# Performance work log

Measured on AMD Instinct MI355X. Metric: run time of the kernel, lower is better.

## Reference

```python
import jax, jax.numpy as jnp
import numpy as np

N, E = 50000, 800000
IN, HID, OUT, HEADS = 128, 64, 32, 2


def setup_inputs() -> dict:
    key = jax.random.key(0)
    ks = jax.random.split(key, 16)
    def w(k, shape, fan_in):
        return jax.random.normal(k, shape, dtype=jnp.float32) / np.sqrt(fan_in).astype(np.float32)
    x = jax.random.normal(ks[0], (N, IN), dtype=jnp.float32)
    edge_index = jax.random.randint(ks[1], (2, E), 0, N)
    return {
        "x": x,
        "edge_index": edge_index,
        # GCNConv 1: in -> hid
        "W1": w(ks[2], (IN, HID), IN), "b1": jnp.zeros((HID,), jnp.float32),
        # GCNConv 2: hid -> hid
        "W2": w(ks[3], (HID, HID), HID), "b2": jnp.zeros((HID,), jnp.float32),
        # GATConv 1: hid -> hid, heads=2, concat=True
        "Wg1": w(ks[4], (HID, HEADS * HID), HID),
        "asrc1": w(ks[5], (HEADS, HID), HID), "adst1": w(ks[6], (HEADS, HID), HID),
        "bg1": jnp.zeros((HEADS * HID,), jnp.float32),
        # GATConv 2: hid*2 -> out, heads=2, concat=False (mean over heads)
        "Wg2": w(ks[7], (HEADS * HID, HEADS * OUT), HEADS * HID),
        "asrc2": w(ks[8], (HEADS, OUT), OUT), "adst2": w(ks[9], (HEADS, OUT), OUT),
        "bg2": jnp.zeros((OUT,), jnp.float32),
    }


def _add_self_loops(edge_index, n):
    loop = jnp.arange(n, dtype=edge_index.dtype)
    src = jnp.concatenate([edge_index[0], loop])
    dst = jnp.concatenate([edge_index[1], loop])
    return src, dst


def _gcn_conv(x, W, b, src, dst, n):
    # PyG GCNConv: symmetric normalization with self-loops (already appended).
    h = x @ W  # [N, C]
    deg = jax.ops.segment_sum(jnp.ones(src.shape, jnp.float32), dst, num_segments=n)
    dinv = jnp.where(deg > 0, jax.lax.rsqrt(deg), 0.0)
    norm = dinv[src] * dinv[dst]                       # [E']
    out = jax.ops.segment_sum(h[src] * norm[:, None], dst, num_segments=n)
    return out + b


def _gat_conv(x, W, a_src, a_dst, bias, src, dst, n, heads, ch, concat):
    # PyG GATConv: per-edge LeakyReLU score, softmax over incoming edges of dst.
    h = (x @ W).reshape(n, heads, ch)                  # [N, H, C]
    s = jnp.sum(h * a_src, axis=-1)                    # [N, H]
    d = jnp.sum(h * a_dst, axis=-1)                    # [N, H]
    e = jax.nn.leaky_relu(s[src] + d[dst], negative_slope=0.2)  # [E', H]
    m = jax.ops.segment_max(e, dst, num_segments=n)    # segment-softmax, stable
    a = jnp.exp(e - m[dst])
    z = jax.ops.segment_sum(a, dst, num_segments=n)
    a = a / (z[dst] + 1e-16)
    out = jax.ops.segment_sum(h[src] * a[:, :, None], dst, num_segments=n)  # [N, H, C]
    out = out.reshape(n, heads * ch) if concat else out.mean(axis=1)
    return out + bias


def reference(x, edge_index, W1, b1, W2, b2, Wg1, asrc1, adst1, bg1, Wg2, asrc2, adst2, bg2):
    n = x.shape[0]
    src, dst = _add_self_loops(edge_index, n)
    h = jax.nn.relu(_gcn_conv(x, W1, b1, src, dst, n))
    h = jax.nn.relu(_gcn_conv(h, W2, b2, src, dst, n))
    h = jax.nn.relu(_gat_conv(h, Wg1, asrc1, adst1, bg1, src, dst, n, HEADS, HID, True))
    h = _gat_conv(h, Wg2, asrc2, adst2, bg2, src, dst, n, HEADS, OUT, False)
    return jax.nn.log_softmax(h, axis=1)
```

## Files before the change

kernel.cpp:

```cpp
#include <hip/hip_runtime.h>
#include <hip/hip_bf16.h>

typedef __hip_bfloat16 bf16;
typedef __attribute__((ext_vector_type(8))) short bf16x8;
typedef __attribute__((ext_vector_type(4))) float f32x4;

constexpr int NN = 50000;
constexpr int NE = 800000;
constexpr int NT = NE + NN;
constexpr int NNB  = (NN + 127)/128;
constexpr int NPART = 8;
constexpr int PCAP = 512;

__device__ __forceinline__ float cvt(const void* p, long long i, int f32){
  return f32 ? ((const float*)p)[i] : __bfloat162float(((const bf16*)p)[i]);
}
__device__ __forceinline__ unsigned short f2bf(float f){
  unsigned u = __float_as_uint(f);
  u += 0x7fffu + ((u >> 16) & 1);
  return (unsigned short)(u >> 16);
}
__device__ __forceinline__ float bflo(unsigned p){ return __uint_as_float(p << 16); }
__device__ __forceinline__ float bfhi(unsigned p){ return __uint_as_float(p & 0xffff0000u); }
__device__ __forceinline__ unsigned packbf(float a, float b){
  return (unsigned)f2bf(a) | ((unsigned)f2bf(b) << 16);
}
__device__ __forceinline__ unsigned f2key(float f){
  unsigned u = __float_as_uint(f);
  return (u & 0x80000000u) ? ~u : (u | 0x80000000u);
}
__device__ __forceinline__ float key2f(unsigned k){
  unsigned u = (k & 0x80000000u) ? (k & 0x7fffffffu) : ~k;
  return __uint_as_float(u);
}

struct SrcPtrs { const void* p[12]; };
__global__ void k_cvtall(SrcPtrs sp, float* __restrict__ Wc,
                         unsigned short* __restrict__ Wf, int* __restrict__ flag){
  const int sz[12]  = {8192,64,4096,64,8192,128,128,128,8192,64,64,32};
  const int off[12] = {0,8192,8256,12352,12416,20608,20736,20864,20992,29184,29248,29312};
  __shared__ int bad;
  int tid = threadIdx.x;
  if(tid == 0) bad = 0;
  __syncthreads();
  const unsigned short* q = (const unsigned short*)sp.p[0];
  int local = 0;
  for(int i = tid; i < 8192; i += 256){
    int e = (q[i] >> 7) & 0xFF;
    if(e >= 0xC0) local = 1;
  }
  if(local) atomicOr(&bad, 1);
  __syncthreads();
  int f = bad;
  int b = blockIdx.x;
  if(b == 0 && tid == 0) *flag = f;
  if(b < 12){
    const void* src = sp.p[b];
    float* dst = Wc + off[b];
    int n = sz[b];
    for(int i = tid; i < n; i += 256) dst[i] = cvt(src, i, f);
  } else {
    int g = b - 12;
    const int KK[4]   = {128, 64, 64, 128};
    const int NNo[4]  = {64, 64, 128, 64};
    const int srcI[4] = {0, 2, 4, 8};
    const int foff[4] = {0, 16384, 24576, 40960};
    int K = KK[g], N = NNo[g], KF = K/32;
    const void* src = sp.p[srcI[g]];
    unsigned short* dh = Wf + foff[g];
    unsigned short* dl = dh + K*N;
    int tot = K*N;
    for(int idx = tid; idx < tot; idx += 256){
      int i = idx & 7, lane = (idx >> 3) & 63, fr = idx >> 9;
      int kf = fr % KF, nf = fr / KF;
      int k = kf*32 + ((lane >> 4) << 3) + i;
      int n = nf*16 + (lane & 15);
      float w = cvt(src, (long long)k*N + n, f);
      unsigned short h = f2bf(w);
      dh[idx] = h;
      dl[idx] = f2bf(w - __uint_as_float((unsigned)h << 16));
    }
  }
}

__global__ void k_bin(const int* __restrict__ ei, int* __restrict__ bcur,
                      unsigned* __restrict__ tmp){
  int e = blockIdx.x*256 + threadIdx.x;
  int p = blockIdx.x & (NPART-1);
  if(e < NE){
    int dst = ei[NE + e];
    int src = ei[e];
    int b = dst >> 7;
    int pos = atomicAdd(&bcur[(p*NNB + b)*16], 1);
    if(pos < PCAP) tmp[((size_t)(b*NPART + p) << 9) + pos] = (unsigned)src | ((unsigned)(dst & 127) << 16);
  }
}
__global__ void k_scatter(const int* __restrict__ bcur,
                          const unsigned* __restrict__ tmp, int* __restrict__ rowptr,
                          int* __restrict__ rowend, float* __restrict__ dinv,
                          unsigned short* __restrict__ srcidx16){
  __shared__ int hist[128];
  __shared__ int lcur[128];
  __shared__ int sh[2][128];
  __shared__ int red[256];
  int b = blockIdx.x;
  int dst0 = b << 7;
  int nd = min(128, NN - dst0);
  int tid = threadIdx.x;
  int partial = 0;
  for(int i = tid; i < b*NPART; i += 256){
    int b2 = i >> 3, p = i & 7;
    partial += bcur[(p*NNB + b2)*16];
  }
  red[tid] = partial;
  if(tid < 128) hist[tid] = 0;
  __syncthreads();
  for(int off = 128; off; off >>= 1){
    if(tid < off) red[tid] += red[tid + off];
    __syncthreads();
  }
  int base = red[0] + (b << 7);
  for(int p = 0; p < NPART; p++){
    int cnt = min(bcur[(p*NNB + b)*16], PCAP);
    const unsigned* tp = tmp + ((size_t)(b*NPART + p) << 9);
    for(int i = tid; i < cnt; i += 256) atomicAdd(&hist[tp[i] >> 16], 1);
  }
  __syncthreads();
  int c = (tid < 128) ? hist[tid] + 1 : 0;
  if(tid < 128) sh[0][tid] = c;
  __syncthreads();
  int cur = 0;
  for(int off = 1; off < 128; off <<= 1){
    int nxt = cur^1;
    if(tid < 128){
      int v = sh[cur][tid];
      if(tid >= off) v += sh[cur][tid-off];
      sh[nxt][tid] = v;
    }
    __syncthreads();
    cur = nxt;
  }
  if(tid < nd){
    int rp = base + sh[cur][tid] - c;
    int d = dst0 + tid;
    rowptr[d] = rp;
    srcidx16[rp] = (unsigned short)d;
    rowend[d] = rp + c;
    dinv[d] = rsqrtf((float)c);
    lcur[tid] = rp + 1;
  }
  __syncthreads();
  for(int p = 0; p < NPART; p++){
    int cnt = min(bcur[(p*NNB + b)*16], PCAP);
    const unsigned* tp = tmp + ((size_t)(b*NPART + p) << 9);
    for(int i = tid; i < cnt; i += 256){
      unsigned v = tp[i];
      int pos = atomicAdd(&lcur[v >> 16], 1);
      srcidx16[pos] = (unsigned short)(v & 0xffffu);
    }
  }
}

template<int KIN, int KOUT, bool SCALE, int PACKC, int MODE>
__global__ void k_mfma(const void* __restrict__ X, const unsigned short* __restrict__ Wh,
                       const unsigned short* __restrict__ Wl,
                       const float* __restrict__ dinv, void* __restrict__ out,
                       const float* __restrict__ asrc, const float* __restrict__ adst,
                       float* __restrict__ sS, float* __restrict__ sD,
                       unsigned* __restrict__ ska, const int* __restrict__ flag){
  constexpr int KF = KIN/32;
  constexpr int NF = KOUT/16;
  constexpr int PITCH = KOUT + 1;
  __shared__ float Cl[64*PITCH];
  __shared__ unsigned skey[2];
  int tid = threadIdx.x;
  if(PACKC > 0 && tid < 2) skey[tid] = 0;
  int wv = tid >> 6, lane = tid & 63;
  int lr = lane >> 4, lc = lane & 15;
  int row0 = blockIdx.x*64;
  int arow = row0 + wv*16 + lc;
  if(arow >= NN) arow = NN - 1;
  int f = (MODE == 1) ? *flag : 0;
  const char* xb = (const char*)X;
  f32x4 acc[NF];
#pragma unroll
  for(int nf = 0; nf < NF; nf++) acc[nf] = (f32x4){0.f,0.f,0.f,0.f};
#pragma unroll
  for(int kf = 0; kf < KF; kf++){
    bf16x8 a;
    if(MODE == 1 && f){
      const float* xf = (const float*)xb + (size_t)arow*KIN + kf*32 + lr*8;
      float4 u = *(const float4*)xf;
      float4 v = *(const float4*)(xf + 4);
      a[0]=(short)f2bf(u.x); a[1]=(short)f2bf(u.y); a[2]=(short)f2bf(u.z); a[3]=(short)f2bf(u.w);
      a[4]=(short)f2bf(v.x); a[5]=(short)f2bf(v.y); a[6]=(short)f2bf(v.z); a[7]=(short)f2bf(v.w);
    } else {
      a = *(const bf16x8*)(xb + (size_t)arow*(KIN*2) + kf*64 + lr*16);
    }
#pragma unroll
    for(int nf = 0; nf < NF; nf++){
      int fr = nf*KF + kf;
      bf16x8 wh = *(const bf16x8*)((const short*)Wh + (fr << 9) + (lane << 3));
      bf16x8 wl = *(const bf16x8*)((const short*)Wl + (fr << 9) + (lane << 3));
      acc[nf] = __builtin_amdgcn_mfma_f32_16x16x32_bf16(a, wh, acc[nf], 0, 0, 0);
      acc[nf] = __builtin_amdgcn_mfma_f32_16x16x32_bf16(a, wl, acc[nf], 0, 0, 0);
    }
  }
#pragma unroll
  for(int nf = 0; nf < NF; nf++)
#pragma unroll
    for(int r = 0; r < 4; r++)
      Cl[(wv*16 + lr*4 + r)*PITCH + nf*16 + lc] = acc[nf][r];
  __syncthreads();
  int row = tid >> 2, q = tid & 3;
  int grow = row0 + row;
  bool valid = grow < NN;
  const float* cr = &Cl[row*PITCH];
  if constexpr (PACKC == 0){
    float s = SCALE ? (valid ? dinv[grow] : 0.0f) : 1.0f;
    unsigned ov[8];
#pragma unroll
    for(int j = 0; j < 8; j++)
      ov[j] = packbf(cr[q*16 + 2*j]*s, cr[q*16 + 2*j + 1]*s);
    if(valid){
      unsigned* op = (unsigned*)out + (size_t)grow*(KOUT/2) + q*8;
      *(uint4*)op       = make_uint4(ov[0],ov[1],ov[2],ov[3]);
      *(uint4*)(op + 4) = make_uint4(ov[4],ov[5],ov[6],ov[7]);
    }
  } else {
    constexpr int C = PACKC;
    constexpr int CT = C/4;
    float s0=0.f, d0=0.f, s1=0.f, d1=0.f;
    unsigned ov[CT];
#pragma unroll
    for(int j = 0; j < CT; j++){
      int c = q*CT + j;
      float a = cr[c], bb = cr[C + c];
      ov[j] = packbf(a, bb);
      s0 += a*asrc[c];      d0 += a*adst[c];
      s1 += bb*asrc[C + c]; d1 += bb*adst[C + c];
    }
    if(valid){
      unsigned* op = (unsigned*)out + (size_t)grow*C + q*CT;
#pragma unroll
      for(int j4 = 0; j4 < CT/4; j4++)
        *(uint4*)(op + 4*j4) = make_uint4(ov[4*j4],ov[4*j4+1],ov[4*j4+2],ov[4*j4+3]);
    }
    s0 += __shfl_xor(s0,1); s0 += __shfl_xor(s0,2);
    d0 += __shfl_xor(d0,1); d0 += __shfl_xor(d0,2);
    s1 += __shfl_xor(s1,1); s1 += __shfl_xor(s1,2);
    d1 += __shfl_xor(d1,1); d1 += __shfl_xor(d1,2);
    if(valid && q == 0){
      *(float2*)(sS + 2*grow) = make_float2(s0, s1);
      *(float2*)(sD + 2*grow) = make_float2(d0, d1);
      atomicMax(&skey[0], f2key(s0));
      atomicMax(&skey[1], f2key(s1));
    }
    __syncthreads();
    if(tid < 2) atomicMax(&ska[tid*32 + (blockIdx.x & 31)], skey[tid]);
  }
}

__global__ void k_gcn_gather(const int* __restrict__ rowptr, const int* __restrict__ rowend,
                             const unsigned short* __restrict__ srcidx16, const float* __restrict__ dinv,
                             const unsigned* __restrict__ Au32, const float* __restrict__ bias,
                             unsigned* __restrict__ B){
  int wid = threadIdx.x >> 6, lane = threadIdx.x & 63;
  int n = blockIdx.x*4 + wid;
  if(n >= NN) return;
  int s0 = rowptr[n], ne = rowend[n] - s0;
  int o = lane >> 3, c4 = lane & 7;
  float a0=0,a1=0,a2=0,a3=0,a4=0,a5=0,a6=0,a7=0;
  for(int base = 0; base < ne; base += 64){
    int my = base + lane;
    int src = (my < ne) ? (int)srcidx16[s0 + my] : -1;
    int cnt = min(64, ne - base);
    int iters = (cnt + 7) >> 3;
#pragma unroll 4
    for(int j = 0; j < iters; j++){
      int sb = __shfl(src, 8*j + o);
      if(sb >= 0){
        uint4 p = *(const uint4*)(Au32 + (size_t)sb*32 + c4*4);
        a0 += bflo(p.x); a1 += bfhi(p.x);
        a2 += bflo(p.y); a3 += bfhi(p.y);
        a4 += bflo(p.z); a5 += bfhi(p.z);
        a6 += bflo(p.w); a7 += bfhi(p.w);
      }
    }
  }
#pragma unroll
  for(int off = 8; off <= 32; off <<= 1){
    a0 += __shfl_xor(a0, off); a1 += __shfl_xor(a1, off);
    a2 += __shfl_xor(a2, off); a3 += __shfl_xor(a3, off);
    a4 += __shfl_xor(a4, off); a5 += __shfl_xor(a5, off);
    a6 += __shfl_xor(a6, off); a7 += __shfl_xor(a7, off);
  }
  if(o == 0){
    float dn = dinv[n];
    int cb = 8*c4;
    uint4 r;
    r.x = packbf(fmaxf(a0*dn + bias[cb+0], 0.0f), fmaxf(a1*dn + bias[cb+1], 0.0f));
    r.y = packbf(fmaxf(a2*dn + bias[cb+2], 0.0f), fmaxf(a3*dn + bias[cb+3], 0.0f));
    r.z = packbf(fmaxf(a4*dn + bias[cb+4], 0.0f), fmaxf(a5*dn + bias[cb+5], 0.0f));
    r.w = packbf(fmaxf(a6*dn + bias[cb+6], 0.0f), fmaxf(a7*dn + bias[cb+7], 0.0f));
    *(uint4*)(B + (size_t)n*32 + c4*4) = r;
  }
}

__device__ __forceinline__ void ska_max2(const unsigned* __restrict__ ska, int lane,
                                         float& m0, float& m1){
  unsigned kk = ska[lane];
#pragma unroll
  for(int off = 1; off <= 16; off <<= 1) kk = max(kk, __shfl_xor(kk, off));
  m0 = key2f(__shfl(kk, 0));
  m1 = key2f(__shfl(kk, 32));
}

__global__ void k_gat1_gather(const int* __restrict__ rowptr, const int* __restrict__ rowend,
                              const unsigned short* __restrict__ srcidx16, const float* __restrict__ sS,
                              const float* __restrict__ sD, const unsigned* __restrict__ Ab,
                              const float* __restrict__ bias, unsigned* __restrict__ B,
                              const unsigned* __restrict__ ska){
  int wid = threadIdx.x >> 6, lane = threadIdx.x & 63;
  int n = blockIdx.x*4 + wid;
  if(n >= NN) return;
  float g0, g1;
  ska_max2(ska, lane, g0, g1);
  int s0 = rowptr[n], ne = rowend[n] - s0;
  float d0 = sD[n*2], d1 = sD[n*2+1];
  float t0 = g0 + d0;  float m0 = t0 > 0.0f ? t0 : 0.2f*t0;
  float t1 = g1 + d1;  float m1 = t1 > 0.0f ? t1 : 0.2f*t1;
  int q = lane >> 4, c4 = lane & 15;
  float z0 = 0.0f, z1 = 0.0f;
  float b0=0,b1=0,b2=0,b3=0, c0=0,c1=0,c2=0,c3=0;
  for(int base = 0; base < ne; base += 64){
    int my = base + lane;
    int src = 0; float w0 = 0.0f, w1 = 0.0f;
    if(my < ne){
      src = (int)srcidx16[s0 + my];
      float2 sv = *(const float2*)(sS + src*2);
      float e0 = sv.x + d0; e0 = e0 > 0.0f ? e0 : 0.2f*e0;
      float e1 = sv.y + d1; e1 = e1 > 0.0f ? e1 : 0.2f*e1;
      w0 = __expf(e0 - m0); w1 = __expf(e1 - m1);
      z0 += w0; z1 += w1;
    }
    int cnt = min(64, ne - base);
    int iters = (cnt + 3) >> 2;
#pragma unroll 4
    for(int j = 0; j < iters; j++){
      int idx = 4*j + q;
      int sb = __shfl(src, idx);
      float a0 = __shfl(w0, idx), a1 = __shfl(w1, idx);
      uint4 p = *(const uint4*)(Ab + (size_t)sb*64 + c4*4);
      b0 += bflo(p.x)*a0; c0 += bfhi(p.x)*a1;
      b1 += bflo(p.y)*a0; c1 += bfhi(p.y)*a1;
      b2 += bflo(p.z)*a0; c2 += bfhi(p.z)*a1;
      b3 += bflo(p.w)*a0; c3 += bfhi(p.w)*a1;
    }
  }
#pragma unroll
  for(int off = 1; off <= 32; off <<= 1){ z0 += __shfl_xor(z0, off); z1 += __shfl_xor(z1, off); }
#pragma unroll
  for(int off = 16; off <= 32; off <<= 1){
    b0 += __shfl_xor(b0, off); b1 += __shfl_xor(b1, off);
    b2 += __shfl_xor(b2, off); b3 += __shfl_xor(b3, off);
    c0 += __shfl_xor(c0, off); c1 += __shfl_xor(c1, off);
    c2 += __shfl_xor(c2, off); c3 += __shfl_xor(c3, off);
  }
  if(q == 0){
    float iz0 = 1.0f/(z0 + 1e-16f), iz1 = 1.0f/(z1 + 1e-16f);
    int cb = 4*c4;
    uint2 r0, r1;
    r0.x = packbf(fmaxf(b0*iz0 + bias[cb+0], 0.0f), fmaxf(b1*iz0 + bias[cb+1], 0.0f));
    r0.y = packbf(fmaxf(b2*iz0 + bias[cb+2], 0.0f), fmaxf(b3*iz0 + bias[cb+3], 0.0f));
    r1.x = packbf(fmaxf(c0*iz1 + bias[64+cb+0], 0.0f), fmaxf(c1*iz1 + bias[64+cb+1], 0.0f));
    r1.y = packbf(fmaxf(c2*iz1 + bias[64+cb+2], 0.0f), fmaxf(c3*iz1 + bias[64+cb+3], 0.0f));
    *(uint2*)(B + (size_t)n*64 + 2*c4)      = r0;
    *(uint2*)(B + (size_t)n*64 + 32 + 2*c4) = r1;
  }
}

__global__ void k_gat2_final(const int* __restrict__ rowptr, const int* __restrict__ rowend,
                             const unsigned short* __restrict__ srcidx16, const float* __restrict__ sS,
                             const float* __restrict__ sD, const unsigned* __restrict__ Ab,
                             const float* __restrict__ bias, void* __restrict__ out,
                             const int* __restrict__ flag, const unsigned* __restrict__ ska){
  int wid = threadIdx.x >> 6, lane = threadIdx.x & 63;
  int n = blockIdx.x*4 + wid;
  if(n >= NN) return;
  float g0, g1;
  ska_max2(ska, lane, g0, g1);
  int s0 = rowptr[n], ne = rowend[n] - s0;
  float d0 = sD[n*2], d1 = sD[n*2+1];
  float t0 = g0 + d0;  float m0 = t0 > 0.0f ? t0 : 0.2f*t0;
  float t1 = g1 + d1;  float m1 = t1 > 0.0f ? t1 : 0.2f*t1;
  int o = lane >> 3, c4 = lane & 7;
  float z0 = 0.0f, z1 = 0.0f;
  float b0=0,b1=0,b2=0,b3=0, c0=0,c1=0,c2=0,c3=0;
  for(int base = 0; base < ne; base += 64){
    int my = base + lane;
    int src = 0; float w0 = 0.0f, w1 = 0.0f;
    if(my < ne){
      src = (int)srcidx16[s0 + my];
      float2 sv = *(const float2*)(sS + src*2);
      float e0 = sv.x + d0; e0 = e0 > 0.0f ? e0 : 0.2f*e0;
      float e1 = sv.y + d1; e1 = e1 > 0.0f ? e1 : 0.2f*e1;
      w0 = __expf(e0 - m0); w1 = __expf(e1 - m1);
      z0 += w0; z1 += w1;
    }
    int cnt = min(64, ne - base);
    int iters = (cnt + 7) >> 3;
#pragma unroll 4
    for(int j = 0; j < iters; j++){
      int idx = 8*j + o;
      int sb = __shfl(src, idx);
      float a0 = __shfl(w0, idx), a1 = __shfl(w1, idx);
      uint4 p = *(const uint4*)(Ab + (size_t)sb*32 + c4*4);
      b0 += bflo(p.x)*a0; c0 += bfhi(p.x)*a1;
      b1 += bflo(p.y)*a0; c1 += bfhi(p.y)*a1;
      b2 += bflo(p.z)*a0; c2 += bfhi(p.z)*a1;
      b3 += bflo(p.w)*a0; c3 += bfhi(p.w)*a1;
    }
  }
#pragma unroll
  for(int off = 1; off <= 32; off <<= 1){ z0 += __shfl_xor(z0, off); z1 += __shfl_xor(z1, off); }
#pragma unroll
  for(int off = 8; off <= 32; off <<= 1){
    b0 += __shfl_xor(b0, off); b1 += __shfl_xor(b1, off);
    b2 += __shfl_xor(b2, off); b3 += __shfl_xor(b3, off);
    c0 += __shfl_xor(c0, off); c1 += __shfl_xor(c1, off);
    c2 += __shfl_xor(c2, off); c3 += __shfl_xor(c3, off);
  }
  float iz0 = 1.0f/(z0 + 1e-16f), iz1 = 1.0f/(z1 + 1e-16f);
  int cb = 4*c4;
  float o0 = 0.5f*(b0*iz0 + c0*iz1) + bias[cb+0];
  float o1 = 0.5f*(b1*iz0 + c1*iz1) + bias[cb+1];
  float o2 = 0.5f*(b2*iz0 + c2*iz1) + bias[cb+2];
  float o3 = 0.5f*(b3*iz0 + c3*iz1) + bias[cb+3];
  float mx = fmaxf(fmaxf(o0, o1), fmaxf(o2, o3));
  for(int off = 4; off; off >>= 1) mx = fmaxf(mx, __shfl_xor(mx, off));
  float sm = __expf(o0 - mx) + __expf(o1 - mx) + __expf(o2 - mx) + __expf(o3 - mx);
  for(int off = 4; off; off >>= 1) sm += __shfl_xor(sm, off);
  float lse = mx + __logf(sm);
  if(o == 0){
    if(*flag){
      float4 r;
      r.x = o0 - lse; r.y = o1 - lse; r.z = o2 - lse; r.w = o3 - lse;
      *(float4*)((float*)out + (size_t)n*32 + cb) = r;
    } else {
      uint2 r;
      r.x = packbf(o0 - lse, o1 - lse);
      r.y = packbf(o2 - lse, o3 - lse);
      *(uint2*)((unsigned*)out + (size_t)n*16 + 2*c4) = r;
    }
  }
}

extern "C" void kernel_launch(void* const* d_in, const int* in_sizes, int n_in,
                              void* d_out, int out_size, void* d_ws, size_t ws_size,
                              hipStream_t stream) {
  const void* x   = d_in[0];
  const int*  ei  = (const int*)d_in[1];

  float* A    = (float*)d_ws;
  unsigned short* Au = (unsigned short*)A;
  unsigned* Au32 = (unsigned*)A;
  unsigned* Ab = (unsigned*)(A + (size_t)NN*64);
  float* B    = A + (size_t)NN*128;
  float* dinv = B + (size_t)NN*128;
  float* sS   = dinv + NN;
  float* sD   = sS + 2*NN;
  int* rowptr = (int*)(sD + 2*NN);
  int* rowend = rowptr + NN;
  unsigned short* srcidx16 = (unsigned short*)(rowend + NN);
  unsigned* SKA = (unsigned*)(srcidx16 + NT + 2);
  int* bcur   = (int*)(SKA + 128);
  unsigned* tmp = (unsigned*)(bcur + NPART*NNB*16);
  float* Wc   = (float*)(tmp + (size_t)NNB*NPART*PCAP);
  int*  flag  = (int*)(Wc + 29344);
  uintptr_t wfp = ((uintptr_t)(flag + 1) + 15) & ~(uintptr_t)15;
  unsigned short* Wf = (unsigned short*)wfp;

  const float* b1c  = Wc + 8192;
  const float* b2c  = Wc + 12352;
  const float* as1c = Wc + 20608;
  const float* ad1c = Wc + 20736;
  const float* bg1c = Wc + 20864;
  const float* as2c = Wc + 29184;
  const float* ad2c = Wc + 29248;
  const float* bg2c = Wc + 29312;

  auto nb = [](long long t){ return dim3((unsigned)((t + 255)/256)); };
  dim3 gnodes((NN + 3)/4);
  dim3 g64((NN + 63)/64);

  SrcPtrs sp;
  for(int i = 0; i < 12; i++) sp.p[i] = d_in[2 + i];
  k_cvtall<<<16, 256, 0, stream>>>(sp, Wc, Wf, flag);

  (void)hipMemsetAsync(SKA, 0, 512 + NPART*NNB*16*4, stream);

  k_bin<<<nb(NE), 256, 0, stream>>>(ei, bcur, tmp);
  k_scatter<<<NNB, 256, 0, stream>>>(bcur, tmp, rowptr, rowend, dinv, srcidx16);

  k_mfma<128,64,true,0,1><<<g64, 256, 0, stream>>>(
      x, Wf, Wf + 8192, dinv, Au, nullptr, nullptr, nullptr, nullptr, nullptr, flag);
  k_gcn_gather<<<gnodes, 256, 0, stream>>>(rowptr, rowend, srcidx16, dinv, Au32, b1c, (unsigned*)B);

  k_mfma<64,64,true,0,0><<<g64, 256, 0, stream>>>(
      B, Wf + 16384, Wf + 20480, dinv, Au, nullptr, nullptr, nullptr, nullptr, nullptr, flag);
  k_gcn_gather<<<gnodes, 256, 0, stream>>>(rowptr, rowend, srcidx16, dinv, Au32, b2c, (unsigned*)B);

  k_mfma<64,128,false,64,0><<<g64, 256, 0, stream>>>(
      B, Wf + 24576, Wf + 32768, dinv, Ab, as1c, ad1c, sS, sD, SKA, flag);
  k_gat1_gather<<<gnodes, 256, 0, stream>>>(rowptr, rowend, srcidx16, sS, sD, Ab, bg1c, (unsigned*)B, SKA);

  k_mfma<128,64,false,32,0><<<g64, 256, 0, stream>>>(
      B, Wf + 40960, Wf + 49152, dinv, Ab, as2c, ad2c, sS, sD, SKA + 64, flag);
  k_gat2_final<<<gnodes, 256, 0, stream>>>(rowptr, rowend, srcidx16, sS, sD, Ab, bg2c, d_out, flag, SKA + 64);
}
```

Measured before the change: 346.1 us.

## Process multiple nodes per wavefront in gather kernels and fold memset into cvt kernel

Each wavefront in the GCN gather kernel now handles 4 destination nodes, and each wavefront in the two GAT gather kernels handles 2. Their neighbor index loads are issued up front and the first 64 edges go through fully unrolled loops, so more independent memory loads are in flight per wave. The hipMemsetAsync is replaced by extra blocks in the weight-conversion kernel that zero the same buffers, removing one launch. The cost is higher register pressure and fewer waves in total, which may reduce occupancy and latency hiding.

Measured after the change: 351.3 us. Within noise of the previous version (+1.5%).

```diff
diff --git a/kernel.cpp b/kernel.cpp
--- a/kernel.cpp
+++ b/kernel.cpp
@@ -36,11 +36,18 @@
 
 struct SrcPtrs { const void* p[12]; };
 __global__ void k_cvtall(SrcPtrs sp, float* __restrict__ Wc,
-                         unsigned short* __restrict__ Wf, int* __restrict__ flag){
+                         unsigned short* __restrict__ Wf, int* __restrict__ flag,
+                         unsigned* __restrict__ zero0){
   const int sz[12]  = {8192,64,4096,64,8192,128,128,128,8192,64,64,32};
   const int off[12] = {0,8192,8256,12352,12416,20608,20736,20864,20992,29184,29248,29312};
+  int tid = threadIdx.x;
+  int b = blockIdx.x;
+  if(b >= 16){
+    constexpr int ZN = 128 + NPART*NNB*16;
+    for(int i = (b-16)*256 + tid; i < ZN; i += 8*256) zero0[i] = 0u;
+    return;
+  }
   __shared__ int bad;
-  int tid = threadIdx.x;
   if(tid == 0) bad = 0;
   __syncthreads();
   const unsigned short* q = (const unsigned short*)sp.p[0];
@@ -52,7 +59,6 @@
   if(local) atomicOr(&bad, 1);
   __syncthreads();
   int f = bad;
-  int b = blockIdx.x;
   if(b == 0 && tid == 0) *flag = f;
   if(b < 12){
     const void* src = sp.p[b];
@@ -266,44 +272,78 @@
                              const unsigned* __restrict__ Au32, const float* __restrict__ bias,
                              unsigned* __restrict__ B){
   int wid = threadIdx.x >> 6, lane = threadIdx.x & 63;
-  int n = blockIdx.x*4 + wid;
-  if(n >= NN) return;
-  int s0 = rowptr[n], ne = rowend[n] - s0;
+  int n0 = (blockIdx.x*4 + wid)*4;
+  if(n0 >= NN) return;
   int o = lane >> 3, c4 = lane & 7;
-  float a0=0,a1=0,a2=0,a3=0,a4=0,a5=0,a6=0,a7=0;
-  for(int base = 0; base < ne; base += 64){
-    int my = base + lane;
-    int src = (my < ne) ? (int)srcidx16[s0 + my] : -1;
-    int cnt = min(64, ne - base);
-    int iters = (cnt + 7) >> 3;
-#pragma unroll 4
-    for(int j = 0; j < iters; j++){
-      int sb = __shfl(src, 8*j + o);
+  int s0[4], ne[4], src[4];
+  float acc[4][8];
+#pragma unroll
+  for(int i = 0; i < 4; i++){
+    int n = min(n0 + i, NN-1);
+    s0[i] = rowptr[n]; ne[i] = rowend[n] - s0[i];
+    if(n0 + i >= NN) ne[i] = 0;
+#pragma unroll
+    for(int c = 0; c < 8; c++) acc[i][c] = 0.f;
+  }
+#pragma unroll
+  for(int i = 0; i < 4; i++)
+    src[i] = (lane < ne[i]) ? (int)srcidx16[s0[i] + lane] : -1;
+#pragma unroll
+  for(int i = 0; i < 4; i++){
+#pragma unroll
+    for(int j = 0; j < 8; j++){
+      if(j*8 >= ne[i]) break;
+      int sb = __shfl(src[i], 8*j + o);
       if(sb >= 0){
         uint4 p = *(const uint4*)(Au32 + (size_t)sb*32 + c4*4);
-        a0 += bflo(p.x); a1 += bfhi(p.x);
-        a2 += bflo(p.y); a3 += bfhi(p.y);
-        a4 += bflo(p.z); a5 += bfhi(p.z);
-        a6 += bflo(p.w); a7 += bfhi(p.w);
+        acc[i][0] += bflo(p.x); acc[i][1] += bfhi(p.x);
+        acc[i][2] += bflo(p.y); acc[i][3] += bfhi(p.y);
+        acc[i][4] += bflo(p.z); acc[i][5] += bfhi(p.z);
+        acc[i][6] += bflo(p.w); acc[i][7] += bfhi(p.w);
       }
     }
   }
 #pragma unroll
-  for(int off = 8; off <= 32; off <<= 1){
-    a0 += __shfl_xor(a0, off); a1 += __shfl_xor(a1, off);
-    a2 += __shfl_xor(a2, off); a3 += __shfl_xor(a3, off);
-    a4 += __shfl_xor(a4, off); a5 += __shfl_xor(a5, off);
-    a6 += __shfl_xor(a6, off); a7 += __shfl_xor(a7, off);
-  }
+  for(int i = 0; i < 4; i++){
+    for(int base = 64; base < ne[i]; base += 64){
+      int my = base + lane;
+      int s = (my < ne[i]) ? (int)srcidx16[s0[i] + my] : -1;
+      int iters = (min(64, ne[i] - base) + 7) >> 3;
+      for(int j = 0; j < iters; j++){
+        int sb = __shfl(s, 8*j + o);
+        if(sb >= 0){
+          uint4 p = *(const uint4*)(Au32 + (size_t)sb*32 + c4*4);
+          acc[i][0] += bflo(p.x); acc[i][1] += bfhi(p.x);
+          acc[i][2] += bflo(p.y); acc[i][3] += bfhi(p.y);
+          acc[i][4] += bflo(p.z); acc[i][5] += bfhi(p.z);
+          acc[i][6] += bflo(p.w); acc[i][7] += bfhi(p.w);
+        }
+      }
+    }
+  }
+#pragma unroll
+  for(int i = 0; i < 4; i++)
+#pragma unroll
+    for(int off = 8; off <= 32; off <<= 1){
+      acc[i][0] += __shfl_xor(acc[i][0], off); acc[i][1] += __shfl_xor(acc[i][1], off);
+      acc[i][2] += __shfl_xor(acc[i][2], off); acc[i][3] += __shfl_xor(acc[i][3], off);
+      acc[i][4] += __shfl_xor(acc[i][4], off); acc[i][5] += __shfl_xor(acc[i][5], off);
+      acc[i][6] += __shfl_xor(acc[i][6], off); acc[i][7] += __shfl_xor(acc[i][7], off);
+    }
   if(o == 0){
-    float dn = dinv[n];
     int cb = 8*c4;
-    uint4 r;
-    r.x = packbf(fmaxf(a0*dn + bias[cb+0], 0.0f), fmaxf(a1*dn + bias[cb+1], 0.0f));
-    r.y = packbf(fmaxf(a2*dn + bias[cb+2], 0.0f), fmaxf(a3*dn + bias[cb+3], 0.0f));
-    r.z = packbf(fmaxf(a4*dn + bias[cb+4], 0.0f), fmaxf(a5*dn + bias[cb+5], 0.0f));
-    r.w = packbf(fmaxf(a6*dn + bias[cb+6], 0.0f), fmaxf(a7*dn + bias[cb+7], 0.0f));
-    *(uint4*)(B + (size_t)n*32 + c4*4) = r;
+#pragma unroll
+    for(int i = 0; i < 4; i++){
+      int n = n0 + i;
+      if(n >= NN) break;
+      float dn = dinv[n];
+      uint4 r;
+      r.x = packbf(fmaxf(acc[i][0]*dn + bias[cb+0], 0.0f), fmaxf(acc[i][1]*dn + bias[cb+1], 0.0f));
+      r.y = packbf(fmaxf(acc[i][2]*dn + bias[cb+2], 0.0f), fmaxf(acc[i][3]*dn + bias[cb+3], 0.0f));
+      r.z = packbf(fmaxf(acc[i][4]*dn + bias[cb+4], 0.0f), fmaxf(acc[i][5]*dn + bias[cb+5], 0.0f));
+      r.w = packbf(fmaxf(acc[i][6]*dn + bias[cb+6], 0.0f), fmaxf(acc[i][7]*dn + bias[cb+7], 0.0f));
+      *(uint4*)(B + (size_t)n*32 + c4*4) = r;
+    }
   }
 }
 
@@ -322,61 +362,106 @@
                               const float* __restrict__ bias, unsigned* __restrict__ B,
                               const unsigned* __restrict__ ska){
   int wid = threadIdx.x >> 6, lane = threadIdx.x & 63;
-  int n = blockIdx.x*4 + wid;
-  if(n >= NN) return;
+  int n0 = (blockIdx.x*4 + wid)*2;
+  if(n0 >= NN) return;
   float g0, g1;
   ska_max2(ska, lane, g0, g1);
-  int s0 = rowptr[n], ne = rowend[n] - s0;
-  float d0 = sD[n*2], d1 = sD[n*2+1];
-  float t0 = g0 + d0;  float m0 = t0 > 0.0f ? t0 : 0.2f*t0;
-  float t1 = g1 + d1;  float m1 = t1 > 0.0f ? t1 : 0.2f*t1;
   int q = lane >> 4, c4 = lane & 15;
-  float z0 = 0.0f, z1 = 0.0f;
-  float b0=0,b1=0,b2=0,b3=0, c0=0,c1=0,c2=0,c3=0;
-  for(int base = 0; base < ne; base += 64){
-    int my = base + lane;
-    int src = 0; float w0 = 0.0f, w1 = 0.0f;
-    if(my < ne){
-      src = (int)srcidx16[s0 + my];
-      float2 sv = *(const float2*)(sS + src*2);
-      float e0 = sv.x + d0; e0 = e0 > 0.0f ? e0 : 0.2f*e0;
-      float e1 = sv.y + d1; e1 = e1 > 0.0f ? e1 : 0.2f*e1;
-      w0 = __expf(e0 - m0); w1 = __expf(e1 - m1);
-      z0 += w0; z1 += w1;
-    }
-    int cnt = min(64, ne - base);
-    int iters = (cnt + 3) >> 2;
-#pragma unroll 4
-    for(int j = 0; j < iters; j++){
+  int s0[2], ne[2], src[2];
+  float d0[2], d1[2], m0[2], m1[2], w0[2], w1[2];
+  float z0[2] = {0.f,0.f}, z1[2] = {0.f,0.f};
+  float ab[2][4], ac[2][4];
+#pragma unroll
+  for(int i = 0; i < 2; i++){
+    int n = min(n0 + i, NN-1);
+    s0[i] = rowptr[n]; ne[i] = rowend[n] - s0[i];
+    if(n0 + i >= NN) ne[i] = 0;
+    d0[i] = sD[n*2]; d1[i] = sD[n*2+1];
+    float t0 = g0 + d0[i];  m0[i] = t0 > 0.0f ? t0 : 0.2f*t0;
+    float t1 = g1 + d1[i];  m1[i] = t1 > 0.0f ? t1 : 0.2f*t1;
+#pragma unroll
+    for(int c = 0; c < 4; c++){ ab[i][c] = 0.f; ac[i][c] = 0.f; }
+  }
+#pragma unroll
+  for(int i = 0; i < 2; i++){
+    src[i] = 0; w0[i] = 0.f; w1[i] = 0.f;
+    if(lane < ne[i]){
+      src[i] = (int)srcidx16[s0[i] + lane];
+      float2 sv = *(const float2*)(sS + src[i]*2);
+      float e0 = sv.x + d0[i]; e0 = e0 > 0.0f ? e0 : 0.2f*e0;
+      float e1 = sv.y + d1[i]; e1 = e1 > 0.0f ? e1 : 0.2f*e1;
+      w0[i] = __expf(e0 - m0[i]); w1[i] = __expf(e1 - m1[i]);
+      z0[i] += w0[i]; z1[i] += w1[i];
+    }
+  }
+#pragma unroll
+  for(int i = 0; i < 2; i++){
+#pragma unroll
+    for(int j = 0; j < 16; j++){
+      if(4*j >= ne[i]) break;
       int idx = 4*j + q;
-      int sb = __shfl(src, idx);
-      float a0 = __shfl(w0, idx), a1 = __shfl(w1, idx);
+      int sb = __shfl(src[i], idx);
+      float a0 = __shfl(w0[i], idx), a1 = __shfl(w1[i], idx);
       uint4 p = *(const uint4*)(Ab + (size_t)sb*64 + c4*4);
-      b0 += bflo(p.x)*a0; c0 += bfhi(p.x)*a1;
-      b1 += bflo(p.y)*a0; c1 += bfhi(p.y)*a1;
-      b2 += bflo(p.z)*a0; c2 += bfhi(p.z)*a1;
-      b3 += bflo(p.w)*a0; c3 += bfhi(p.w)*a1;
-    }
-  }
-#pragma unroll
-  for(int off = 1; off <= 32; off <<= 1){ z0 += __shfl_xor(z0, off); z1 += __shfl_xor(z1, off); }
-#pragma unroll
-  for(int off = 16; off <= 32; off <<= 1){
-    b0 += __shfl_xor(b0, off); b1 += __shfl_xor(b1, off);
-    b2 += __shfl_xor(b2, off); b3 += __shfl_xor(b3, off);
-    c0 += __shfl_xor(c0, off); c1 += __shfl_xor(c1, off);
-    c2 += __shfl_xor(c2, off); c3 += __shfl_xor(c3, off);
+      ab[i][0] += bflo(p.x)*a0; ac[i][0] += bfhi(p.x)*a1;
+      ab[i][1] += bflo(p.y)*a0; ac[i][1] += bfhi(p.y)*a1;
+      ab[i][2] += bflo(p.z)*a0; ac[i][2] += bfhi(p.z)*a1;
+      ab[i][3] += bflo(p.w)*a0; ac[i][3] += bfhi(p.w)*a1;
+    }
+  }
+#pragma unroll
+  for(int i = 0; i < 2; i++){
+    for(int base = 64; base < ne[i]; base += 64){
+      int my = base + lane;
+      int s = 0; float u0 = 0.f, u1 = 0.f;
+      if(my < ne[i]){
+        s = (int)srcidx16[s0[i] + my];
+        float2 sv = *(const float2*)(sS + s*2);
+        float e0 = sv.x + d0[i]; e0 = e0 > 0.0f ? e0 : 0.2f*e0;
+        float e1 = sv.y + d1[i]; e1 = e1 > 0.0f ? e1 : 0.2f*e1;
+        u0 = __expf(e0 - m0[i]); u1 = __expf(e1 - m1[i]);
+        z0[i] += u0; z1[i] += u1;
+      }
+      int iters = (min(64, ne[i] - base) + 3) >> 2;
+      for(int j = 0; j < iters; j++){
+        int idx = 4*j + q;
+        int sb = __shfl(s, idx);
+        float a0 = __shfl(u0, idx), a1 = __shfl(u1, idx);
+        uint4 p = *(const uint4*)(Ab + (size_t)sb*64 + c4*4);
+        ab[i][0] += bflo(p.x)*a0; ac[i][0] += bfhi(p.x)*a1;
+        ab[i][1] += bflo(p.y)*a0; ac[i][1] += bfhi(p.y)*a1;
+        ab[i][2] += bflo(p.z)*a0; ac[i][2] += bfhi(p.z)*a1;
+        ab[i][3] += bflo(p.w)*a0; ac[i][3] += bfhi(p.w)*a1;
+      }
+    }
+  }
+#pragma unroll
+  for(int i = 0; i < 2; i++){
+#pragma unroll
+    for(int off = 1; off <= 32; off <<= 1){ z0[i] += __shfl_xor(z0[i], off); z1[i] += __shfl_xor(z1[i], off); }
+#pragma unroll
+    for(int off = 16; off <= 32; off <<= 1){
+      ab[i][0] += __shfl_xor(ab[i][0], off); ab[i][1] += __shfl_xor(ab[i][1], off);
+      ab[i][2] += __shfl_xor(ab[i][2], off); ab[i][3] += __shfl_xor(ab[i][3], off);
+      ac[i][0] += __shfl_xor(ac[i][0], off); ac[i][1] += __shfl_xor(ac[i][1], off);
+      ac[i][2] += __shfl_xor(ac[i][2], off); ac[i][3] += __shfl_xor(ac[i][3], off);
+    }
   }
   if(q == 0){
-    float iz0 = 1.0f/(z0 + 1e-16f), iz1 = 1.0f/(z1 + 1e-16f);
     int cb = 4*c4;
-    uint2 r0, r1;
-    r0.x = packbf(fmaxf(b0*iz0 + bias[cb+0], 0.0f), fmaxf(b1*iz0 + bias[cb+1], 0.0f));
-    r0.y = packbf(fmaxf(b2*iz0 + bias[cb+2], 0.0f), fmaxf(b3*iz0 + bias[cb+3], 0.0f));
-    r1.x = packbf(fmaxf(c0*iz1 + bias[64+cb+0], 0.0f), fmaxf(c1*iz1 + bias[64+cb+1], 0.0f));
-    r1.y = packbf(fmaxf(c2*iz1 + bias[64+cb+2], 0.0f), fmaxf(c3*iz1 + bias[64+cb+3], 0.0f));
-    *(uint2*)(B + (size_t)n*64 + 2*c4)      = r0;
-    *(uint2*)(B + (size_t)n*64 + 32 + 2*c4) = r1;
+#pragma unroll
+    for(int i = 0; i < 2; i++){
+      int n = n0 + i;
+      if(n >= NN) break;
+      float iz0 = 1.0f/(z0[i] + 1e-16f), iz1 = 1.0f/(z1[i] + 1e-16f);
+      uint2 r0, r1;
+      r0.x = packbf(fmaxf(ab[i][0]*iz0 + bias[cb+0], 0.0f), fmaxf(ab[i][1]*iz0 + bias[cb+1], 0.0f));
+      r0.y = packbf(fmaxf(ab[i][2]*iz0 + bias[cb+2], 0.0f), fmaxf(ab[i][3]*iz0 + bias[cb+3], 0.0f));
+      r1.x = packbf(fmaxf(ac[i][0]*iz1 + bias[64+cb+0], 0.0f), fmaxf(ac[i][1]*iz1 + bias[64+cb+1], 0.0f));
+      r1.y = packbf(fmaxf(ac[i][2]*iz1 + bias[64+cb+2], 0.0f), fmaxf(ac[i][3]*iz1 + bias[64+cb+3], 0.0f));
+      *(uint2*)(B + (size_t)n*64 + 2*c4)      = r0;
+      *(uint2*)(B + (size_t)n*64 + 32 + 2*c4) = r1;
+    }
   }
 }
 
@@ -386,72 +471,115 @@
                              const float* __restrict__ bias, void* __restrict__ out,
                              const int* __restrict__ flag, const unsigned* __restrict__ ska){
   int wid = threadIdx.x >> 6, lane = threadIdx.x & 63;
-  int n = blockIdx.x*4 + wid;
-  if(n >= NN) return;
+  int n0 = (blockIdx.x*4 + wid)*2;
+  if(n0 >= NN) return;
   float g0, g1;
   ska_max2(ska, lane, g0, g1);
-  int s0 = rowptr[n], ne = rowend[n] - s0;
-  float d0 = sD[n*2], d1 = sD[n*2+1];
-  float t0 = g0 + d0;  float m0 = t0 > 0.0f ? t0 : 0.2f*t0;
-  float t1 = g1 + d1;  float m1 = t1 > 0.0f ? t1 : 0.2f*t1;
   int o = lane >> 3, c4 = lane & 7;
-  float z0 = 0.0f, z1 = 0.0f;
-  float b0=0,b1=0,b2=0,b3=0, c0=0,c1=0,c2=0,c3=0;
-  for(int base = 0; base < ne; base += 64){
-    int my = base + lane;
-    int src = 0; float w0 = 0.0f, w1 = 0.0f;
-    if(my < ne){
-      src = (int)srcidx16[s0 + my];
-      float2 sv = *(const float2*)(sS + src*2);
-      float e0 = sv.x + d0; e0 = e0 > 0.0f ? e0 : 0.2f*e0;
-      float e1 = sv.y + d1; e1 = e1 > 0.0f ? e1 : 0.2f*e1;
-      w0 = __expf(e0 - m0); w1 = __expf(e1 - m1);
-      z0 += w0; z1 += w1;
-    }
-    int cnt = min(64, ne - base);
-    int iters = (cnt + 7) >> 3;
-#pragma unroll 4
-    for(int j = 0; j < iters; j++){
+  int s0[2], ne[2], src[2];
+  float d0[2], d1[2], m0[2], m1[2], w0[2], w1[2];
+  float z0[2] = {0.f,0.f}, z1[2] = {0.f,0.f};
+  float ab[2][4], ac[2][4];
+#pragma unroll
+  for(int i = 0; i < 2; i++){
+    int n = min(n0 + i, NN-1);
+    s0[i] = rowptr[n]; ne[i] = rowend[n] - s0[i];
+    if(n0 + i >= NN) ne[i] = 0;
+    d0[i] = sD[n*2]; d1[i] = sD[n*2+1];
+    float t0 = g0 + d0[i];  m0[i] = t0 > 0.0f ? t0 : 0.2f*t0;
+    float t1 = g1 + d1[i];  m1[i] = t1 > 0.0f ? t1 : 0.2f*t1;
+#pragma unroll
+    for(int c = 0; c < 4; c++){ ab[i][c] = 0.f; ac[i][c] = 0.f; }
+  }
+#pragma unroll
+  for(int i = 0; i < 2; i++){
+    src[i] = 0; w0[i] = 0.f; w1[i] = 0.f;
+    if(lane < ne[i]){
+      src[i] = (int)srcidx16[s0[i] + lane];
+      float2 sv = *(const float2*)(sS + src[i]*2);
+      float e0 = sv.x + d0[i]; e0 = e0 > 0.0f ? e0 : 0.2f*e0;
+      float e1 = sv.y + d1[i]; e1 = e1 > 0.0f ? e1 : 0.2f*e1;
+      w0[i] = __expf(e0 - m0[i]); w1[i] = __expf(e1 - m1[i]);
+      z0[i] += w0[i]; z1[i] += w1[i];
+    }
+  }
+#pragma unroll
+  for(int i = 0; i < 2; i++){
+#pragma unroll
+    for(int j = 0; j < 8; j++){
+      if(8*j >= ne[i]) break;
       int idx = 8*j + o;
-      int sb = __shfl(src, idx);
-      float a0 = __shfl(w0, idx), a1 = __shfl(w1, idx);
+      int sb = __shfl(src[i], idx);
+      float a0 = __shfl(w0[i], idx), a1 = __shfl(w1[i], idx);
       uint4 p = *(const uint4*)(Ab + (size_t)sb*32 + c4*4);
-      b0 += bflo(p.x)*a0; c0 += bfhi(p.x)*a1;
-      b1 += bflo(p.y)*a0; c1 += bfhi(p.y)*a1;
-      b2 += bflo(p.z)*a0; c2 += bfhi(p.z)*a1;
-      b3 += bflo(p.w)*a0; c3 += bfhi(p.w)*a1;
-    }
-  }
-#pragma unroll
-  for(int off = 1; off <= 32; off <<= 1){ z0 += __shfl_xor(z0, off); z1 += __shfl_xor(z1, off); }
-#pragma unroll
-  for(int off = 8; off <= 32; off <<= 1){
-    b0 += __shfl_xor(b0, off); b1 += __shfl_xor(b1, off);
-    b2 += __shfl_xor(b2, off); b3 += __shfl_xor(b3, off);
-    c0 += __shfl_xor(c0, off); c1 += __shfl_xor(c1, off);
-    c2 += __shfl_xor(c2, off); c3 += __shfl_xor(c3, off);
-  }
-  float iz0 = 1.0f/(z0 + 1e-16f), iz1 = 1.0f/(z1 + 1e-16f);
-  int cb = 4*c4;
-  float o0 = 0.5f*(b0*iz0 + c0*iz1) + bias[cb+0];
-  float o1 = 0.5f*(b1*iz0 + c1*iz1) + bias[cb+1];
-  float o2 = 0.5f*(b2*iz0 + c2*iz1) + bias[cb+2];
-  float o3 = 0.5f*(b3*iz0 + c3*iz1) + bias[cb+3];
-  float mx = fmaxf(fmaxf(o0, o1), fmaxf(o2, o3));
-  for(int off = 4; off; off >>= 1) mx = fmaxf(mx, __shfl_xor(mx, off));
-  float sm = __expf(o0 - mx) + __expf(o1 - mx) + __expf(o2 - mx) + __expf(o3 - mx);
-  for(int off = 4; off; off >>= 1) sm += __shfl_xor(sm, off);
-  float lse = mx + __logf(sm);
-  if(o == 0){
-    if(*flag){
-      float4 r;
-      r.x = o0 - lse; r.y = o1 - lse; r.z = o2 - lse; r.w = o3 - lse;
-      *(float4*)((float*)out + (size_t)n*32 + cb) = r;
-    } else {
-      uint2 r;
-      r.x = packbf(o0 - lse, o1 - lse);
-      r.y = packbf(o2 - lse, o3 - lse);
-      *(uint2*)((unsigned*)out + (size_t)n*16 + 2*c4) = r;
+      ab[i][0] += bflo(p.x)*a0; ac[i][0] += bfhi(p.x)*a1;
+      ab[i][1] += bflo(p.y)*a0; ac[i][1] += bfhi(p.y)*a1;
+      ab[i][2] += bflo(p.z)*a0; ac[i][2] += bfhi(p.z)*a1;
+      ab[i][3] += bflo(p.w)*a0; ac[i][3] += bfhi(p.w)*a1;
+    }
+  }
+#pragma unroll
+  for(int i = 0; i < 2; i++){
+    for(int base = 64; base < ne[i]; base += 64){
+      int my = base + lane;
+      int s = 0; float u0 = 0.f, u1 = 0.f;
+      if(my < ne[i]){
+        s = (int)srcidx16[s0[i] + my];
+        float2 sv = *(const float2*)(sS + s*2);
+        float e0 = sv.x + d0[i]; e0 = e0 > 0.0f ? e0 : 0.2f*e0;
+        float e1 = sv.y + d1[i]; e1 = e1 > 0.0f ? e1 : 0.2f*e1;
+        u0 = __expf(e0 - m0[i]); u1 = __expf(e1 - m1[i]);
+        z0[i] += u0; z1[i] += u1;
+      }
+      int iters = (min(64, ne[i] - base) + 7) >> 3;
+      for(int j = 0; j < iters; j++){
+        int idx = 8*j + o;
+        int sb = __shfl(s, idx);
+        float a0 = __shfl(u0, idx), a1 = __shfl(u1, idx);
+        uint4 p = *(const uint4*)(Ab + (size_t)sb*32 + c4*4);
+        ab[i][0] += bflo(p.x)*a0; ac[i][0] += bfhi(p.x)*a1;
+        ab[i][1] += bflo(p.y)*a0; ac[i][1] += bfhi(p.y)*a1;
+        ab[i][2] += bflo(p.z)*a0; ac[i][2] += bfhi(p.z)*a1;
+        ab[i][3] += bflo(p.w)*a0; ac[i][3] += bfhi(p.w)*a1;
+      }
+    }
+  }
+  int fl = *flag;
+#pragma unroll
+  for(int i = 0; i < 2; i++){
+#pragma unroll
+    for(int off = 1; off <= 32; off <<= 1){ z0[i] += __shfl_xor(z0[i], off); z1[i] += __shfl_xor(z1[i], off); }
+#pragma unroll
+    for(int off = 8; off <= 32; off <<= 1){
+      ab[i][0] += __shfl_xor(ab[i][0], off); ab[i][1] += __shfl_xor(ab[i][1], off);
+      ab[i][2] += __shfl_xor(ab[i][2], off); ab[i][3] += __shfl_xor(ab[i][3], off);
+      ac[i][0] += __shfl_xor(ac[i][0], off); ac[i][1] += __shfl_xor(ac[i][1], off);
+      ac[i][2] += __shfl_xor(ac[i][2], off); ac[i][3] += __shfl_xor(ac[i][3], off);
+    }
+    int n = n0 + i;
+    if(n >= NN) continue;
+    float iz0 = 1.0f/(z0[i] + 1e-16f), iz1 = 1.0f/(z1[i] + 1e-16f);
+    int cb = 4*c4;
+    float o0 = 0.5f*(ab[i][0]*iz0 + ac[i][0]*iz1) + bias[cb+0];
+    float o1 = 0.5f*(ab[i][1]*iz0 + ac[i][1]*iz1) + bias[cb+1];
+    float o2 = 0.5f*(ab[i][2]*iz0 + ac[i][2]*iz1) + bias[cb+2];
+    float o3 = 0.5f*(ab[i][3]*iz0 + ac[i][3]*iz1) + bias[cb+3];
+    float mx = fmaxf(fmaxf(o0, o1), fmaxf(o2, o3));
+    for(int off = 4; off; off >>= 1) mx = fmaxf(mx, __shfl_xor(mx, off));
+    float sm = __expf(o0 - mx) + __expf(o1 - mx) + __expf(o2 - mx) + __expf(o3 - mx);
+    for(int off = 4; off; off >>= 1) sm += __shfl_xor(sm, off);
+    float lse = mx + __logf(sm);
+    if(o == 0){
+      if(fl){
+        float4 r;
+        r.x = o0 - lse; r.y = o1 - lse; r.z = o2 - lse; r.w = o3 - lse;
+        *(float4*)((float*)out + (size_t)n*32 + cb) = r;
+      } else {
+        uint2 r;
+        r.x = packbf(o0 - lse, o1 - lse);
+        r.y = packbf(o2 - lse, o3 - lse);
+        *(uint2*)((unsigned*)out + (size_t)n*16 + 2*c4) = r;
+      }
     }
   }
 }
@@ -491,31 +619,30 @@
   const float* bg2c = Wc + 29312;
 
   auto nb = [](long long t){ return dim3((unsigned)((t + 255)/256)); };
-  dim3 gnodes((NN + 3)/4);
+  dim3 g16((NN + 15)/16);
+  dim3 g8((NN + 7)/8);
   dim3 g64((NN + 63)/64);
 
   SrcPtrs sp;
   for(int i = 0; i < 12; i++) sp.p[i] = d_in[2 + i];
-  k_cvtall<<<16, 256, 0, stream>>>(sp, Wc, Wf, flag);
-
-  (void)hipMemsetAsync(SKA, 0, 512 + NPART*NNB*16*4, stream);
+  k_cvtall<<<24, 256, 0, stream>>>(sp, Wc, Wf, flag, SKA);
 
   k_bin<<<nb(NE), 256, 0, stream>>>(ei, bcur, tmp);
   k_scatter<<<NNB, 256, 0, stream>>>(bcur, tmp, rowptr, rowend, dinv, srcidx16);
 
   k_mfma<128,64,true,0,1><<<g64, 256, 0, stream>>>(
       x, Wf, Wf + 8192, dinv, Au, nullptr, nullptr, nullptr, nullptr, nullptr, flag);
-  k_gcn_gather<<<gnodes, 256, 0, stream>>>(rowptr, rowend, srcidx16, dinv, Au32, b1c, (unsigned*)B);
+  k_gcn_gather<<<g16, 256, 0, stream>>>(rowptr, rowend, srcidx16, dinv, Au32, b1c, (unsigned*)B);
 
   k_mfma<64,64,true,0,0><<<g64, 256, 0, stream>>>(
       B, Wf + 16384, Wf + 20480, dinv, Au, nullptr, nullptr, nullptr, nullptr, nullptr, flag);
-  k_gcn_gather<<<gnodes, 256, 0, stream>>>(rowptr, rowend, srcidx16, dinv, Au32, b2c, (unsigned*)B);
+  k_gcn_gather<<<g16, 256, 0, stream>>>(rowptr, rowend, srcidx16, dinv, Au32, b2c, (unsigned*)B);
 
   k_mfma<64,128,false,64,0><<<g64, 256, 0, stream>>>(
       B, Wf + 24576, Wf + 32768, dinv, Ab, as1c, ad1c, sS, sD, SKA, flag);
-  k_gat1_gather<<<gnodes, 256, 0, stream>>>(rowptr, rowend, srcidx16, sS, sD, Ab, bg1c, (unsigned*)B, SKA);
+  k_gat1_gather<<<g8, 256, 0, stream>>>(rowptr, rowend, srcidx16, sS, sD, Ab, bg1c, (unsigned*)B, SKA);
 
   k_mfma<128,64,false,32,0><<<g64, 256, 0, stream>>>(
       B, Wf + 40960, Wf + 49152, dinv, Ab, as2c, ad2c, sS, sD, SKA + 64, flag);
-  k_gat2_final<<<gnodes, 256, 0, stream>>>(rowptr, rowend, srcidx16, sS, sD, Ab, bg2c, d_out, flag, SKA + 64);
-}
+  k_gat2_final<<<g8, 256, 0, stream>>>(rowptr, rowend, srcidx16, sS, sD, Ab, bg2c, d_out, flag, SKA + 64);
+}
```
